# Kernel optimization log

Measured on AMD Instinct MI355X. Metric: run time of the kernel, lower is better.

## Reference

```python
import jax, jax.numpy as jnp
import numpy as np

R, T, D = 512, 512, 256   # robots, tasks, per-entity embedding dim
INPUT_DIM = 2 * D         # 512
HIDDEN_DIM = 512


def setup_inputs() -> dict:
    key = jax.random.key(0)
    k1, k2, k3, k4, k5, k6 = jax.random.split(key, 6)
    lim1 = 1.0 / np.sqrt(INPUT_DIM)
    lim2 = 1.0 / np.sqrt(HIDDEN_DIM)
    return {
        "robot_embeddings": jax.random.normal(k1, (R, D), dtype=jnp.float32),
        "task_embeddings": jax.random.normal(k2, (T, D), dtype=jnp.float32),
        "W1": jax.random.uniform(k3, (INPUT_DIM, HIDDEN_DIM), jnp.float32, -lim1, lim1),
        "b1": jax.random.uniform(k4, (HIDDEN_DIM,), jnp.float32, -lim1, lim1),
        "W2": jax.random.uniform(k5, (HIDDEN_DIM, 1), jnp.float32, -lim2, lim2),
        "b2": jax.random.uniform(k6, (1,), jnp.float32, -lim2, lim2),
    }


def reference(robot_embeddings, task_embeddings, W1, b1, W2, b2):
    # Equivalent to the nested loop: for each (robot, task) pair,
    # mlp(concat([robot, task])) -> scalar; output [R, T].
    # Split W1 into the robot half and the task half so we never
    # materialize the [R, T, 2D] concatenated tensor:
    #   concat(r, t) @ W1 == r @ W1[:D] + t @ W1[D:]
    rpart = robot_embeddings @ W1[:D]          # [R, H]
    tpart = task_embeddings @ W1[D:]           # [T, H]
    h = jax.nn.relu(rpart[:, None, :] + tpart[None, :, :] + b1)  # [R, T, H]
    scores = jnp.einsum("rth,ho->rt", h, W2) + b2[0]             # [R, T]
    return scores
```

## Files before the change

### kernel.cpp

```cpp
#include <hip/hip_runtime.h>
#include <hip/hip_fp16.h>


#define RT 512
#define DD 256
#define HD 512

typedef _Float16 h2 __attribute__((ext_vector_type(2)));
typedef _Float16 h8 __attribute__((ext_vector_type(8)));
typedef float f32x4 __attribute__((ext_vector_type(4)));

__device__ inline unsigned h2u(h2 v) { return __builtin_bit_cast(unsigned, v); }
__device__ inline h2 u2h(unsigned u) { return __builtin_bit_cast(h2, u); }
__device__ inline h2 pk(float a, float b) {
    return __builtin_bit_cast(h2, __builtin_amdgcn_cvt_pkrtz(a, b));
}

__global__ __launch_bounds__(256) void gemm_fused(
    const float* __restrict__ robot, const float* __restrict__ task,
    const float* __restrict__ W1, const float* __restrict__ b1,
    float* __restrict__ ws)
{
    __shared__ __attribute__((aligned(16))) unsigned short As[32 * 256];
    __shared__ __attribute__((aligned(16))) unsigned short Bs[64 * 256];

    const int z = blockIdx.z;
    const int mtile = blockIdx.y * 32;
    const int ntile = blockIdx.x * 64;
    const int tid = threadIdx.x;
    const int wave = tid >> 6, lane = tid & 63;

    const float* A = z ? task : robot;

    #pragma unroll
    for (int it = 0; it < 4; ++it) {
        int idx = tid + 256 * it;
        int m = idx >> 5, k8 = idx & 31;
        const float* src = &A[(mtile + m) * DD + k8 * 8];
        float4 v0 = *(const float4*)src;
        float4 v1 = *(const float4*)(src + 4);
        uint4 o = make_uint4(h2u(pk(v0.x, v0.y)), h2u(pk(v0.z, v0.w)),
                             h2u(pk(v1.x, v1.y)), h2u(pk(v1.z, v1.w)));
        *(uint4*)((char*)As + ((m * 512 + k8 * 16) ^ ((m & 7) << 4))) = o;
    }

    {
        const float* Wz = W1 + z * DD * HD;
        #pragma unroll
        for (int k8 = 0; k8 < 8; ++k8) {
            int k0 = wave * 64 + k8 * 8;
            float f[8];
            #pragma unroll
            for (int u = 0; u < 8; ++u)
                f[u] = Wz[(k0 + u) * HD + ntile + lane];
            uint4 o = make_uint4(h2u(pk(f[0], f[1])), h2u(pk(f[2], f[3])),
                                 h2u(pk(f[4], f[5])), h2u(pk(f[6], f[7])));
            *(uint4*)((char*)Bs + ((lane * 512 + k0 * 2) ^ ((lane & 7) << 4))) = o;
        }
    }
    __syncthreads();

    const int wn = wave * 16;
    const int lm = lane & 15;
    const int lkb = (lane >> 4) * 16;

    f32x4 acc0 = {0.f, 0.f, 0.f, 0.f}, acc1 = {0.f, 0.f, 0.f, 0.f};
    #pragma unroll
    for (int ks = 0; ks < 8; ++ks) {
        int rb = wn + lm;
        h8 b  = *(const h8*)((const char*)Bs + ((rb * 512 + ks * 64 + lkb) ^ ((rb & 7) << 4)));
        h8 a0 = *(const h8*)((const char*)As + ((lm * 512 + ks * 64 + lkb) ^ ((lm & 7) << 4)));
        h8 a1 = *(const h8*)((const char*)As + (((16 + lm) * 512 + ks * 64 + lkb) ^ ((lm & 7) << 4)));
        acc0 = __builtin_amdgcn_mfma_f32_16x16x32_f16(a0, b, acc0, 0, 0, 0);
        acc1 = __builtin_amdgcn_mfma_f32_16x16x32_f16(a1, b, acc1, 0, 0, 0);
    }

    float* outT = ws + z * (RT * RT);
    const int h = ntile + wn + lm;
    const float bias = (z == 0) ? b1[h] : 0.f;
    const int rrow = (lane >> 4) * 4;
    *(float4*)&outT[h * RT + mtile + rrow] =
        make_float4(acc0[0] + bias, acc0[1] + bias, acc0[2] + bias, acc0[3] + bias);
    *(float4*)&outT[h * RT + mtile + 16 + rrow] =
        make_float4(acc1[0] + bias, acc1[1] + bias, acc1[2] + bias, acc1[3] + bias);
}

__global__ __launch_bounds__(512) void score(
    const float* __restrict__ ws, const float* __restrict__ W2,
    const float* __restrict__ b2, float* __restrict__ out)
{
    __shared__ __attribute__((aligned(16))) unsigned smem[16384];
    unsigned* rs = smem;
    unsigned* ts = smem + 8192;

    const float* rpT = ws;
    const float* tpT = ws + RT * RT;
    const int tid = threadIdx.x;
    const int rbase = blockIdx.y * 32, tbase = blockIdx.x * 32;

    #pragma unroll
    for (int i = 0; i < 8; ++i) {
        int u = tid + 512 * i;
        int hp = (u >> 3) & 255;
        int rq = (u & 7) * 4;
        if (u < 2048) {
            float4 v0 = *(const float4*)&rpT[(2 * hp) * RT + rbase + rq];
            float4 v1 = *(const float4*)&rpT[(2 * hp + 1) * RT + rbase + rq];
            *(uint4*)&rs[hp * 32 + rq] = make_uint4(
                h2u(pk(v0.x, v1.x)), h2u(pk(v0.y, v1.y)),
                h2u(pk(v0.z, v1.z)), h2u(pk(v0.w, v1.w)));
        } else {
            float4 v0 = *(const float4*)&tpT[(2 * hp) * RT + tbase + rq];
            float4 v1 = *(const float4*)&tpT[(2 * hp + 1) * RT + tbase + rq];
            *(uint4*)&ts[hp * 32 + rq] = make_uint4(
                h2u(pk(v0.x, v1.x)), h2u(pk(v0.y, v1.y)),
                h2u(pk(v0.z, v1.z)), h2u(pk(v0.w, v1.w)));
        }
    }
    __syncthreads();

    const int wave = tid >> 6, lane = tid & 63;
    const int ly = (lane >> 3) & 7, lx = lane & 7;
    const h2 hzero = {};

    float acc[4][4] = {};
    const int s0 = wave * 32;
    #pragma unroll 4
    for (int s = s0; s < s0 + 32; ++s) {
        uint4 da = *(const uint4*)&rs[s * 32 + 4 * ly];
        uint4 dc = *(const uint4*)&ts[s * 32 + 4 * lx];
        float2 wf = *(const float2*)&W2[2 * s];
        h2 wv = pk(wf.x, wf.y);
        h2 a[4] = {u2h(da.x), u2h(da.y), u2h(da.z), u2h(da.w)};
        h2 c[4] = {u2h(dc.x), u2h(dc.y), u2h(dc.z), u2h(dc.w)};
        #pragma unroll
        for (int i2 = 0; i2 < 4; ++i2)
            #pragma unroll
            for (int j2 = 0; j2 < 4; ++j2) {
                h2 p = a[i2] + c[j2];
                p = __builtin_elementwise_max(p, hzero);
                acc[i2][j2] = __builtin_amdgcn_fdot2(p, wv, acc[i2][j2], false);
            }
    }

    __syncthreads();
    float* red = (float*)smem;
    {
        float* p = &red[wave * 1280 + lane * 20];
        #pragma unroll
        for (int i2 = 0; i2 < 4; ++i2)
            *(float4*)&p[4 * i2] = make_float4(acc[i2][0], acc[i2][1], acc[i2][2], acc[i2][3]);
    }
    __syncthreads();
    const float b2v = b2[0];
    #pragma unroll
    for (int half = 0; half < 2; ++half) {
        int j = tid + half * 512;
        float sum = 0.f;
        #pragma unroll
        for (int w = 0; w < 8; ++w) sum += red[w * 1280 + (j >> 4) * 20 + (j & 15)];
        int ly2 = j >> 7, lx2 = (j >> 4) & 7, dr = (j >> 2) & 3, dt = j & 3;
        out[(rbase + 4 * ly2 + dr) * RT + tbase + 4 * lx2 + dt] = sum + b2v;
    }
}

extern "C" void kernel_launch(void* const* d_in, const int* in_sizes, int n_in,
                              void* d_out, int out_size, void* d_ws, size_t ws_size,
                              hipStream_t stream) {
    const float* robot = (const float*)d_in[0];
    const float* task  = (const float*)d_in[1];
    const float* W1    = (const float*)d_in[2];
    const float* b1    = (const float*)d_in[3];
    const float* W2    = (const float*)d_in[4];
    const float* b2    = (const float*)d_in[5];
    float* out = (float*)d_out;
    float* ws  = (float*)d_ws;

    gemm_fused<<<dim3(8, 16, 2), 256, 0, stream>>>(robot, task, W1, b1, ws);
    score<<<dim3(16, 16), 512, 0, stream>>>(ws, W2, b2, out);
}
```

Measured before the change: 19.95 us.

## Store GEMM intermediates as packed fp16 pairs to halve workspace traffic

The projection GEMM now converts its outputs to packed half2 (adjacent hidden units paired) before writing the workspace. The score kernel then loads these directly with no fp32-to-fp16 conversion. The GEMM is also reorganised into a 1D grid of 512-thread blocks: each block covers a 32x64 tile and each wave issues one MFMA, with operand roles swapped so lanes produce hidden-unit pairs. This halves intermediate memory traffic and drops conversion work from the score load phase, at the cost of uncoalesced 4-byte scattered stores in the GEMM epilogue.

```diff
diff --git a/kernel.cpp b/kernel.cpp
--- a/kernel.cpp
+++ b/kernel.cpp
@@ -16,113 +16,96 @@
     return __builtin_bit_cast(h2, __builtin_amdgcn_cvt_pkrtz(a, b));
 }
 
-__global__ __launch_bounds__(256) void gemm_fused(
+__global__ __launch_bounds__(512) void gemm_packed(
     const float* __restrict__ robot, const float* __restrict__ task,
     const float* __restrict__ W1, const float* __restrict__ b1,
-    float* __restrict__ ws)
+    unsigned* __restrict__ wsu)
 {
-    __shared__ __attribute__((aligned(16))) unsigned short As[32 * 256];
-    __shared__ __attribute__((aligned(16))) unsigned short Bs[64 * 256];
+    __shared__ __attribute__((aligned(16))) unsigned smem[12288];
+    unsigned short* Ws = (unsigned short*)smem;
+    unsigned short* Xs = (unsigned short*)(smem + 8192);
 
-    const int z = blockIdx.z;
-    const int mtile = blockIdx.y * 32;
-    const int ntile = blockIdx.x * 64;
     const int tid = threadIdx.x;
     const int wave = tid >> 6, lane = tid & 63;
+    const int b = blockIdx.x;
+    const int z = b >> 7, sub = b & 127;
+    const int rtile = (sub & 15) * 32;
+    const int htile = (sub >> 4) * 64;
+    const float* X = z ? task : robot;
+    const float* Wz = W1 + z * DD * HD;
 
-    const float* A = z ? task : robot;
-
+    {
+        int hh = tid & 63, k0 = (tid >> 6) * 32;
+        float f[32];
+        #pragma unroll
+        for (int u = 0; u < 32; ++u)
+            f[u] = Wz[(k0 + u) * HD + htile + hh];
+        #pragma unroll
+        for (int j = 0; j < 4; ++j) {
+            uint4 o = make_uint4(
+                h2u(pk(f[8*j+0], f[8*j+1])), h2u(pk(f[8*j+2], f[8*j+3])),
+                h2u(pk(f[8*j+4], f[8*j+5])), h2u(pk(f[8*j+6], f[8*j+7])));
+            *(uint4*)((char*)Ws + ((hh * 512 + k0 * 2 + j * 16) ^ ((hh & 7) << 4))) = o;
+        }
+    }
     #pragma unroll
-    for (int it = 0; it < 4; ++it) {
-        int idx = tid + 256 * it;
+    for (int i = 0; i < 2; ++i) {
+        int idx = tid + 512 * i;
         int m = idx >> 5, k8 = idx & 31;
-        const float* src = &A[(mtile + m) * DD + k8 * 8];
-        float4 v0 = *(const float4*)src;
-        float4 v1 = *(const float4*)(src + 4);
+        const float* src = &X[(rtile + m) * DD + k8 * 8];
+        float4 v0 = *(const float4*)src, v1 = *(const float4*)(src + 4);
         uint4 o = make_uint4(h2u(pk(v0.x, v0.y)), h2u(pk(v0.z, v0.w)),
                              h2u(pk(v1.x, v1.y)), h2u(pk(v1.z, v1.w)));
-        *(uint4*)((char*)As + ((m * 512 + k8 * 16) ^ ((m & 7) << 4))) = o;
-    }
-
-    {
-        const float* Wz = W1 + z * DD * HD;
-        #pragma unroll
-        for (int k8 = 0; k8 < 8; ++k8) {
-            int k0 = wave * 64 + k8 * 8;
-            float f[8];
-            #pragma unroll
-            for (int u = 0; u < 8; ++u)
-                f[u] = Wz[(k0 + u) * HD + ntile + lane];
-            uint4 o = make_uint4(h2u(pk(f[0], f[1])), h2u(pk(f[2], f[3])),
-                                 h2u(pk(f[4], f[5])), h2u(pk(f[6], f[7])));
-            *(uint4*)((char*)Bs + ((lane * 512 + k0 * 2) ^ ((lane & 7) << 4))) = o;
-        }
+        *(uint4*)((char*)Xs + ((m * 512 + k8 * 16) ^ ((m & 7) << 4))) = o;
     }
     __syncthreads();
 
-    const int wn = wave * 16;
-    const int lm = lane & 15;
-    const int lkb = (lane >> 4) * 16;
-
-    f32x4 acc0 = {0.f, 0.f, 0.f, 0.f}, acc1 = {0.f, 0.f, 0.f, 0.f};
+    const int wh = (wave & 3) * 16, wr = (wave >> 2) * 16;
+    const int lm = lane & 15, lkb = (lane >> 4) * 16;
+    f32x4 acc = {0.f, 0.f, 0.f, 0.f};
     #pragma unroll
     for (int ks = 0; ks < 8; ++ks) {
-        int rb = wn + lm;
-        h8 b  = *(const h8*)((const char*)Bs + ((rb * 512 + ks * 64 + lkb) ^ ((rb & 7) << 4)));
-        h8 a0 = *(const h8*)((const char*)As + ((lm * 512 + ks * 64 + lkb) ^ ((lm & 7) << 4)));
-        h8 a1 = *(const h8*)((const char*)As + (((16 + lm) * 512 + ks * 64 + lkb) ^ ((lm & 7) << 4)));
-        acc0 = __builtin_amdgcn_mfma_f32_16x16x32_f16(a0, b, acc0, 0, 0, 0);
-        acc1 = __builtin_amdgcn_mfma_f32_16x16x32_f16(a1, b, acc1, 0, 0, 0);
+        int ha = wh + lm, ra = wr + lm;
+        h8 a  = *(const h8*)((const char*)Ws + ((ha * 512 + ks * 64 + lkb) ^ ((ha & 7) << 4)));
+        h8 bb = *(const h8*)((const char*)Xs + ((ra * 512 + ks * 64 + lkb) ^ ((ra & 7) << 4)));
+        acc = __builtin_amdgcn_mfma_f32_16x16x32_f16(a, bb, acc, 0, 0, 0);
     }
-
-    float* outT = ws + z * (RT * RT);
-    const int h = ntile + wn + lm;
-    const float bias = (z == 0) ? b1[h] : 0.f;
-    const int rrow = (lane >> 4) * 4;
-    *(float4*)&outT[h * RT + mtile + rrow] =
-        make_float4(acc0[0] + bias, acc0[1] + bias, acc0[2] + bias, acc0[3] + bias);
-    *(float4*)&outT[h * RT + mtile + 16 + rrow] =
-        make_float4(acc1[0] + bias, acc1[1] + bias, acc1[2] + bias, acc1[3] + bias);
+    const int r  = rtile + wr + lm;
+    const int hq = htile + wh + (lane >> 4) * 4;
+    float4 bv = make_float4(0.f, 0.f, 0.f, 0.f);
+    if (z == 0) bv = *(const float4*)&b1[hq];
+    unsigned* P = wsu + z * (256 * RT);
+    P[((hq >> 1) + 0) * RT + r] = h2u(pk(acc[0] + bv.x, acc[1] + bv.y));
+    P[((hq >> 1) + 1) * RT + r] = h2u(pk(acc[2] + bv.z, acc[3] + bv.w));
 }
 
 __global__ __launch_bounds__(512) void score(
-    const float* __restrict__ ws, const float* __restrict__ W2,
+    const unsigned* __restrict__ wsu, const float* __restrict__ W2,
     const float* __restrict__ b2, float* __restrict__ out)
 {
     __shared__ __attribute__((aligned(16))) unsigned smem[16384];
     unsigned* rs = smem;
     unsigned* ts = smem + 8192;
 
-    const float* rpT = ws;
-    const float* tpT = ws + RT * RT;
+    const unsigned* rpP = wsu;
+    const unsigned* tpP = wsu + 256 * RT;
     const int tid = threadIdx.x;
     const int rbase = blockIdx.y * 32, tbase = blockIdx.x * 32;
 
     #pragma unroll
     for (int i = 0; i < 8; ++i) {
         int u = tid + 512 * i;
-        int hp = (u >> 3) & 255;
-        int rq = (u & 7) * 4;
-        if (u < 2048) {
-            float4 v0 = *(const float4*)&rpT[(2 * hp) * RT + rbase + rq];
-            float4 v1 = *(const float4*)&rpT[(2 * hp + 1) * RT + rbase + rq];
-            *(uint4*)&rs[hp * 32 + rq] = make_uint4(
-                h2u(pk(v0.x, v1.x)), h2u(pk(v0.y, v1.y)),
-                h2u(pk(v0.z, v1.z)), h2u(pk(v0.w, v1.w)));
-        } else {
-            float4 v0 = *(const float4*)&tpT[(2 * hp) * RT + tbase + rq];
-            float4 v1 = *(const float4*)&tpT[(2 * hp + 1) * RT + tbase + rq];
-            *(uint4*)&ts[hp * 32 + rq] = make_uint4(
-                h2u(pk(v0.x, v1.x)), h2u(pk(v0.y, v1.y)),
-                h2u(pk(v0.z, v1.z)), h2u(pk(v0.w, v1.w)));
-        }
+        int hp = (u >> 3) & 255, rq = (u & 7) * 4;
+        if (u < 2048)
+            *(uint4*)&rs[hp * 32 + rq] = *(const uint4*)&rpP[hp * RT + rbase + rq];
+        else
+            *(uint4*)&ts[hp * 32 + rq] = *(const uint4*)&tpP[hp * RT + tbase + rq];
     }
     __syncthreads();
 
     const int wave = tid >> 6, lane = tid & 63;
     const int ly = (lane >> 3) & 7, lx = lane & 7;
     const h2 hzero = {};
-
     float acc[4][4] = {};
     const int s0 = wave * 32;
     #pragma unroll 4
@@ -174,8 +157,8 @@
     const float* W2    = (const float*)d_in[4];
     const float* b2    = (const float*)d_in[5];
     float* out = (float*)d_out;
-    float* ws  = (float*)d_ws;
+    unsigned* wsu = (unsigned*)d_ws;
 
-    gemm_fused<<<dim3(8, 16, 2), 256, 0, stream>>>(robot, task, W1, b1, ws);
-    score<<<dim3(16, 16), 512, 0, stream>>>(ws, W2, b2, out);
+    gemm_packed<<<dim3(256), 512, 0, stream>>>(robot, task, W1, b1, wsu);
+    score<<<dim3(16, 16), 512, 0, stream>>>(wsu, W2, b2, out);
 }
```

New measurement: 18.94 us. 1.05x faster.
